# Performance work log

Measured on AMD Instinct MI355X. Metric: run time of the kernel, lower is better.

Reference implementation:

```python
import jax, jax.numpy as jnp
import numpy as np

N_NODES = 200000


def _gcn_conv(x, W, b, src, dst, n):
    # PyG GCNConv: h = D^{-1/2} (A + I) D^{-1/2} (x @ W) + b
    h = x @ W  # [N, F_out]
    deg = jax.ops.segment_sum(jnp.ones(dst.shape[0], x.dtype), dst, num_segments=n)
    dinv = jnp.where(deg > 0, jax.lax.rsqrt(deg), 0.0)  # deg_inv_sqrt, inf -> 0
    norm = dinv[src] * dinv[dst]  # [E+N]
    msg = h[src] * norm[:, None]  # gather + scale, dominant memory traffic
    out = jax.ops.segment_sum(msg, dst, num_segments=n)
    return out + b


def setup_inputs() -> dict:
    key = jax.random.key(0)
    k1, k2, k3, k4, k5, k6 = jax.random.split(key, 6)
    x = jax.random.normal(k1, (N_NODES, 1), dtype=jnp.float32)
    edge_index = jax.random.randint(k2, (2, 12800000), 0, N_NODES, dtype=jnp.int64)
    # Glorot-style init like PyG GCNConv
    W1 = jax.random.normal(k3, (1, 16), dtype=jnp.float32) * (1.0 / np.sqrt(1))
    b1 = jnp.zeros((16,), dtype=jnp.float32)
    W2 = jax.random.normal(k4, (16, 1), dtype=jnp.float32) * (1.0 / np.sqrt(16))
    b2 = jnp.zeros((1,), dtype=jnp.float32)
    return {"x": x, "edge_index": edge_index, "W1": W1, "b1": b1, "W2": W2, "b2": b2}


def reference(x, edge_index, W1, b1, W2, b2):
    n = x.shape[0]
    # add self-loops once (static edge count: E + N)
    loops = jnp.arange(n, dtype=edge_index.dtype)
    src = jnp.concatenate([edge_index[0], loops])
    dst = jnp.concatenate([edge_index[1], loops])
    h = _gcn_conv(x, W1, b1, src, dst, n)
    h = jax.nn.relu(h)
    out = _gcn_conv(h, W2, b2, src, dst, n)
    return out
```

## Files before the change

kernel.cpp:

```cpp
#include <hip/hip_runtime.h>

#define TPB 256
#define BTPB 1024
#define STPB 512
#define LOG_S 13
#define S (1 << LOG_S)
#define RMAX 32
#define CHUNK 8192
#define MAXC 40
#define SLACK 32768
#define SCALEF 2097152.0f
#define INV_SCALEF (1.0f / 2097152.0f)


__global__ void k_initcur(int* __restrict__ cur, int R, int cap) {
    int t = threadIdx.x;
    if (t < R) cur[t] = t * cap;
}

__global__ __launch_bounds__(BTPB) void k_bin(const int* __restrict__ dst,
                                              const int* __restrict__ src, int e,
                                              int R, int cap,
                                              int* __restrict__ cur,
                                              unsigned* __restrict__ bkt) {
    __shared__ unsigned stage[CHUNK];
    __shared__ int h[RMAX], lofs[RMAX + 1], gbase[RMAX];
    int t = threadIdx.x;
    int b0 = blockIdx.x * CHUNK;
    int m = min(CHUNK, e - b0);
    if (t < RMAX) h[t] = 0;
    __syncthreads();
    unsigned pack[8];
    int rr[8];
    const int4* d4p = (const int4*)(dst + b0);
    const int4* s4p = (const int4*)(src + b0);
    int m4 = m >> 2;
    #pragma unroll
    for (int g = 0; g < 2; g++) {
        int i4 = g * BTPB + t;
        if (i4 < m4) {
            int4 d = d4p[i4];
            int4 s = s4p[i4];
            #pragma unroll
            for (int k = 0; k < 4; k++) {
                int dd = (k == 0) ? d.x : (k == 1) ? d.y : (k == 2) ? d.z : d.w;
                int ss = (k == 0) ? s.x : (k == 1) ? s.y : (k == 2) ? s.z : s.w;
                int r = dd >> LOG_S;
                pack[g * 4 + k] = ((unsigned)(dd - (r << LOG_S)) << 18) | (unsigned)ss;
                int rk = atomicAdd(&h[r], 1);
                rr[g * 4 + k] = (r << 13) | rk;
            }
        } else {
            #pragma unroll
            for (int k = 0; k < 4; k++) rr[g * 4 + k] = -1;
        }
    }
    __syncthreads();
    if (t < 64) {
        int hv = (t < R) ? h[t] : 0;
        int v = hv;
        for (int o = 1; o < 64; o <<= 1) {
            int u = __shfl_up(v, o);
            if (t >= o) v += u;
        }
        if (t < R) lofs[t] = v - hv;
        if (t == R - 1) lofs[R] = v;
        if (t < R && hv > 0) gbase[t] = atomicAdd(&cur[t], hv);
    }
    __syncthreads();
    #pragma unroll
    for (int k = 0; k < 8; k++) {
        if (rr[k] >= 0)
            stage[lofs[rr[k] >> 13] + (rr[k] & 8191)] = pack[k];
    }
    __syncthreads();
    for (int j = t; j < m; j += BTPB) {
        int lo = 0, hi = R;
        while (hi - lo > 1) {
            int mid = (lo + hi) >> 1;
            if (lofs[mid] <= j) lo = mid; else hi = mid;
        }
        int gi = gbase[lo] + (j - lofs[lo]);
        if (gi < (lo + 1) * cap)
            bkt[gi] = stage[j];
    }
}

template <int MODE>
__global__ __launch_bounds__(STPB) void k_scat(const unsigned* __restrict__ bkt,
                                               const int* __restrict__ cur,
                                               int cap,
                                               const float* __restrict__ val,
                                               int* __restrict__ partials, int bpr) {
    __shared__ int acc[S];
    int t = threadIdx.x;
    int r = blockIdx.x / bpr;
    int c = blockIdx.x - r * bpr;
    int4* acc4 = (int4*)acc;
    for (int j = t; j < S / 4; j += STPB) acc4[j] = make_int4(0, 0, 0, 0);
    __syncthreads();
    const unsigned* bk = bkt + (size_t)r * cap;
    int len = min(cur[r] - r * cap, cap);
    int len4 = len >> 2;
    const uint4* bk4 = (const uint4*)bk;
    int stride = bpr * STPB;
    int i0 = c * STPB + t;
    bool h0 = i0 < len4, h1 = (i0 + stride) < len4;
    uint4 p0, p1;
    if (h0) p0 = bk4[i0];
    if (h1) p1 = bk4[i0 + stride];
    int v0x = 1, v0y = 1, v0z = 1, v0w = 1;
    if (MODE == 1 && h0) {
        v0x = (int)rintf(val[p0.x & 0x3FFFFu] * SCALEF);
        v0y = (int)rintf(val[p0.y & 0x3FFFFu] * SCALEF);
        v0z = (int)rintf(val[p0.z & 0x3FFFFu] * SCALEF);
        v0w = (int)rintf(val[p0.w & 0x3FFFFu] * SCALEF);
    }
    int inext = i0 + 2 * stride;
    while (h0) {
        uint4 p2;
        bool h2 = inext < len4;
        if (h2) p2 = bk4[inext];
        int v1x = 1, v1y = 1, v1z = 1, v1w = 1;
        if (MODE == 1 && h1) {
            v1x = (int)rintf(val[p1.x & 0x3FFFFu] * SCALEF);
            v1y = (int)rintf(val[p1.y & 0x3FFFFu] * SCALEF);
            v1z = (int)rintf(val[p1.z & 0x3FFFFu] * SCALEF);
            v1w = (int)rintf(val[p1.w & 0x3FFFFu] * SCALEF);
        }
        atomicAdd(&acc[p0.x >> 18], v0x);
        atomicAdd(&acc[p0.y >> 18], v0y);
        atomicAdd(&acc[p0.z >> 18], v0z);
        atomicAdd(&acc[p0.w >> 18], v0w);
        p0 = p1; h0 = h1;
        p1 = p2; h1 = h2;
        v0x = v1x; v0y = v1y; v0z = v1z; v0w = v1w;
        inext += stride;
    }
    for (int k = (len4 << 2) + c * STPB + t; k < len; k += stride) {
        unsigned p = bk[k];
        if (MODE == 0) atomicAdd(&acc[p >> 18], 1);
        else atomicAdd(&acc[p >> 18], (int)rintf(val[p & 0x3FFFFu] * SCALEF));
    }
    __syncthreads();
    if (MODE == 0) {
        unsigned* o16 = (unsigned*)((unsigned short*)partials + (size_t)blockIdx.x * S);
        const int2* acc2 = (const int2*)acc;
        for (int j = t; j < S / 2; j += STPB) {
            int2 a = acc2[j];
            o16[j] = (unsigned)a.x | ((unsigned)a.y << 16);
        }
    } else {
        int4* out4 = (int4*)(partials + (size_t)blockIdx.x * S);
        for (int j = t; j < S / 4; j += STPB) out4[j] = acc4[j];
    }
}

__device__ __forceinline__ int redp(const int* __restrict__ partials, int i, int bpr) {
    int r = i >> LOG_S;
    int slot = i & (S - 1);
    const int* p = partials + (size_t)r * bpr * S + slot;
    int s = 0;
    #pragma unroll 8
    for (int c = 0; c < bpr; c++) s += p[(size_t)c * S];
    return s;
}

__global__ void k_red_dinv(const int* __restrict__ partials, int bpr,
                           const float* __restrict__ x, float* __restrict__ dinv,
                           float* __restrict__ y, int n) {
    int i2 = blockIdx.x * blockDim.x + threadIdx.x;
    int i = i2 << 1;
    if (i + 1 < n) {
        int r = i >> LOG_S;
        int slot = i & (S - 1);
        const unsigned* pb = (const unsigned*)partials
                             + (size_t)r * bpr * (S / 2) + (slot >> 1);
        int s0 = 0, s1 = 0;
        #pragma unroll 8
        for (int c = 0; c < bpr; c++) {
            unsigned v = pb[(size_t)c * (S / 2)];
            s0 += (int)(v & 0xFFFFu);
            s1 += (int)(v >> 16);
        }
        float d0 = rsqrtf((float)s0 + 1.0f);
        float d1 = rsqrtf((float)s1 + 1.0f);
        float2 xx = *(const float2*)(x + i);
        *(float2*)(dinv + i) = make_float2(d0, d1);
        *(float2*)(y + i) = make_float2(xx.x * d0, xx.y * d1);
    } else if (i < n) {
        int r = i >> LOG_S;
        int slot = i & (S - 1);
        const unsigned short* pb = (const unsigned short*)partials
                                   + (size_t)r * bpr * S + slot;
        int s0 = 0;
        for (int c = 0; c < bpr; c++) s0 += (int)pb[(size_t)c * S];
        float d0 = rsqrtf((float)s0 + 1.0f);
        dinv[i] = d0;
        y[i] = x[i] * d0;
    }
}

__global__ void k_red_node(const int* __restrict__ partials, int bpr,
                           const float* __restrict__ dinv, const float* __restrict__ y,
                           float* __restrict__ z,
                           const float* __restrict__ W1, const float* __restrict__ b1,
                           const float* __restrict__ W2, int n, int f) {
    int q = blockIdx.x * blockDim.x + threadIdx.x;
    int i = q << 2;
    if (i + 3 < n) {
        int r = i >> LOG_S;
        int slot = i & (S - 1);
        const int4* p = (const int4*)(partials + (size_t)r * bpr * S + slot);
        int4 s = make_int4(0, 0, 0, 0);
        #pragma unroll 8
        for (int c = 0; c < bpr; c++) {
            int4 v = p[(size_t)c * (S / 4)];
            s.x += v.x; s.y += v.y; s.z += v.z; s.w += v.w;
        }
        float4 dv = *(const float4*)(dinv + i);
        float4 yy = *(const float4*)(y + i);
        float a0 = dv.x * ((float)s.x * INV_SCALEF + yy.x);
        float a1 = dv.y * ((float)s.y * INV_SCALEF + yy.y);
        float a2 = dv.z * ((float)s.z * INV_SCALEF + yy.z);
        float a3 = dv.w * ((float)s.w * INV_SCALEF + yy.w);
        float c0 = 0.0f, c1 = 0.0f, c2 = 0.0f, c3 = 0.0f;
        for (int j = 0; j < f; j++) {
            float w = W1[j], bb = b1[j], u = W2[j];
            c0 += fmaxf(w * a0 + bb, 0.0f) * u;
            c1 += fmaxf(w * a1 + bb, 0.0f) * u;
            c2 += fmaxf(w * a2 + bb, 0.0f) * u;
            c3 += fmaxf(w * a3 + bb, 0.0f) * u;
        }
        *(float4*)(z + i) = make_float4(c0 * dv.x, c1 * dv.y, c2 * dv.z, c3 * dv.w);
    } else {
        for (int k = i; k < n && k < i + 4; k++) {
            float num = (float)redp(partials, k, bpr) * INV_SCALEF;
            float agg = dinv[k] * (num + y[k]);
            float h2 = 0.0f;
            for (int j = 0; j < f; j++) {
                float h = W1[j] * agg + b1[j];
                h2 += fmaxf(h, 0.0f) * W2[j];
            }
            z[k] = h2 * dinv[k];
        }
    }
}

__global__ void k_red_out(const int* __restrict__ partials, int bpr,
                          const float* __restrict__ dinv, const float* __restrict__ z,
                          const float* __restrict__ b2, float* __restrict__ out, int n) {
    int q = blockIdx.x * blockDim.x + threadIdx.x;
    int i = q << 2;
    if (i + 3 < n) {
        int r = i >> LOG_S;
        int slot = i & (S - 1);
        const int4* p = (const int4*)(partials + (size_t)r * bpr * S + slot);
        int4 s = make_int4(0, 0, 0, 0);
        #pragma unroll 8
        for (int c = 0; c < bpr; c++) {
            int4 v = p[(size_t)c * (S / 4)];
            s.x += v.x; s.y += v.y; s.z += v.z; s.w += v.w;
        }
        float4 dv = *(const float4*)(dinv + i);
        float4 zz = *(const float4*)(z + i);
        float bb = b2[0];
        float4 o;
        o.x = dv.x * ((float)s.x * INV_SCALEF + zz.x) + bb;
        o.y = dv.y * ((float)s.y * INV_SCALEF + zz.y) + bb;
        o.z = dv.z * ((float)s.z * INV_SCALEF + zz.z) + bb;
        o.w = dv.w * ((float)s.w * INV_SCALEF + zz.w) + bb;
        *(float4*)(out + i) = o;
    } else {
        for (int k = i; k < n && k < i + 4; k++) {
            float num = (float)redp(partials, k, bpr) * INV_SCALEF;
            out[k] = dinv[k] * (num + z[k]) + b2[0];
        }
    }
}

__global__ void g_init(float* __restrict__ deg, float* __restrict__ num, int n) {
    int i = blockIdx.x * blockDim.x + threadIdx.x;
    if (i < n) { deg[i] = 1.0f; num[i] = 0.0f; }
}
__global__ void g_deg(const int* __restrict__ dst, float* __restrict__ deg, int e) {
    int i = blockIdx.x * blockDim.x + threadIdx.x;
    if (i < e) atomicAdd(deg + dst[i], 1.0f);
}
__global__ void g_dinv(const float* __restrict__ x, float* __restrict__ dd,
                       float* __restrict__ y, int n) {
    int i = blockIdx.x * blockDim.x + threadIdx.x;
    if (i < n) { float d = rsqrtf(dd[i]); dd[i] = d; y[i] = x[i] * d; }
}
__global__ void g_scatter(const int* __restrict__ src, const int* __restrict__ dst,
                          const float* __restrict__ val, float* __restrict__ num, int e) {
    int i = blockIdx.x * blockDim.x + threadIdx.x;
    if (i < e) atomicAdd(num + dst[i], val[src[i]]);
}
__global__ void g_node(const float* __restrict__ dinv, const float* __restrict__ y,
                       float* __restrict__ num, float* __restrict__ z,
                       const float* __restrict__ W1, const float* __restrict__ b1,
                       const float* __restrict__ W2, int n, int f) {
    int i = blockIdx.x * blockDim.x + threadIdx.x;
    if (i < n) {
        float agg = dinv[i] * (num[i] + y[i]);
        float h2 = 0.0f;
        for (int j = 0; j < f; j++) {
            float h = W1[j] * agg + b1[j];
            h2 += fmaxf(h, 0.0f) * W2[j];
        }
        z[i] = h2 * dinv[i];
        num[i] = 0.0f;
    }
}
__global__ void g_out(const float* __restrict__ dinv, const float* __restrict__ z,
                      const float* __restrict__ num, const float* __restrict__ b2,
                      float* __restrict__ out, int n) {
    int i = blockIdx.x * blockDim.x + threadIdx.x;
    if (i < n) out[i] = dinv[i] * (num[i] + z[i]) + b2[0];
}

extern "C" void kernel_launch(void* const* d_in, const int* in_sizes, int n_in,
                              void* d_out, int out_size, void* d_ws, size_t ws_size,
                              hipStream_t stream) {
    const float* x  = (const float*)d_in[0];
    const int*   ei = (const int*)d_in[1];
    const float* W1 = (const float*)d_in[2];
    const float* b1 = (const float*)d_in[3];
    const float* W2 = (const float*)d_in[4];
    const float* b2 = (const float*)d_in[5];

    int n = in_sizes[0];
    int e = in_sizes[1] / 2;
    int f = in_sizes[2];

    const int* src = ei;
    const int* dst = ei + e;
    float* out = (float*)d_out;

    int R  = (n + S - 1) >> LOG_S;
    int gn = (n + TPB - 1) / TPB;
    size_t words = ws_size / 4;

    size_t o_A   = 0;
    size_t o_B   = o_A + n;
    size_t o_D   = o_B + n;
    size_t o_cur = o_D + n;
    size_t o_bkt = (o_cur + RMAX + 3) & ~(size_t)3;
    int cap = ((e / R) + SLACK + 3) & ~3;
    size_t bkt_w = (size_t)R * cap;
    size_t o_part = o_bkt + bkt_w;

    float* A = (float*)d_ws + o_A;
    float* B = (float*)d_ws + o_B;
    float* D = (float*)d_ws + o_D;
    int*   cur = (int*)d_ws + o_cur;

    int bpr = 0;
    if (R <= RMAX && n <= (1 << 18) && words > o_part) {
        size_t per_c = (size_t)R * S;
        size_t m = (words - o_part) / per_c;
        bpr = (int)(m > MAXC ? MAXC : m);
        while (bpr > 0 && R * bpr > 1024) bpr--;
    }

    if (bpr >= 4) {
        unsigned* bkt = (unsigned*)d_ws + o_bkt;
        int* partials = (int*)d_ws + o_part;
        int gs = R * bpr;
        int gbin = (e + CHUNK - 1) / CHUNK;
        int gn2 = (((n + 1) >> 1) + TPB - 1) / TPB;
        int gn4 = (((n + 3) >> 2) + TPB - 1) / TPB;
        k_initcur<<<1, RMAX, 0, stream>>>(cur, R, cap);
        k_bin<<<gbin, BTPB, 0, stream>>>(dst, src, e, R, cap, cur, bkt);
        k_scat<0><<<gs, STPB, 0, stream>>>(bkt, cur, cap, nullptr, partials, bpr);
        k_red_dinv<<<gn2, TPB, 0, stream>>>(partials, bpr, x, A, B, n);
        k_scat<1><<<gs, STPB, 0, stream>>>(bkt, cur, cap, B, partials, bpr);
        k_red_node<<<gn4, TPB, 0, stream>>>(partials, bpr, A, B, D, W1, b1, W2, n, f);
        k_scat<1><<<gs, STPB, 0, stream>>>(bkt, cur, cap, D, partials, bpr);
        k_red_out<<<gn4, TPB, 0, stream>>>(partials, bpr, A, D, b2, out, n);
    } else {
        float* C = D + n;
        int ge = (e + TPB - 1) / TPB;
        g_init<<<gn, TPB, 0, stream>>>(A, C, n);
        g_deg<<<ge, TPB, 0, stream>>>(dst, A, e);
        g_dinv<<<gn, TPB, 0, stream>>>(x, A, B, n);
        g_scatter<<<ge, TPB, 0, stream>>>(src, dst, B, C, e);
        g_node<<<gn, TPB, 0, stream>>>(A, B, C, D, W1, b1, W2, n, f);
        g_scatter<<<ge, TPB, 0, stream>>>(src, dst, D, C, e);
        g_out<<<gn, TPB, 0, stream>>>(A, D, C, b2, out, n);
    }
}
```

Before: 328.6 us.

## Halve per-range scatter blocks and use scalar per-node reduction kernels

Lowers the cap on scatter blocks per bucket range from 40 to 20, which halves the partial histograms each reducer must sum but gives the scatter phase less parallelism. The node and output reduction kernels drop the int4/float4 four-nodes-per-thread path and use one node per thread with the scalar redp helper. Reduce loop unroll factors rise to 20 to match. The scalar path uses narrower loads but launches more threads to hide latency.

```diff
diff --git a/kernel.cpp b/kernel.cpp
--- a/kernel.cpp
+++ b/kernel.cpp
@@ -7,7 +7,7 @@
 #define S (1 << LOG_S)
 #define RMAX 32
 #define CHUNK 8192
-#define MAXC 40
+#define MAXC 20
 #define SLACK 32768
 #define SCALEF 2097152.0f
 #define INV_SCALEF (1.0f / 2097152.0f)
@@ -161,7 +161,7 @@
     int slot = i & (S - 1);
     const int* p = partials + (size_t)r * bpr * S + slot;
     int s = 0;
-    #pragma unroll 8
+    #pragma unroll 20
     for (int c = 0; c < bpr; c++) s += p[(size_t)c * S];
     return s;
 }
@@ -177,7 +177,7 @@
         const unsigned* pb = (const unsigned*)partials
                              + (size_t)r * bpr * (S / 2) + (slot >> 1);
         int s0 = 0, s1 = 0;
-        #pragma unroll 8
+        #pragma unroll 20
         for (int c = 0; c < bpr; c++) {
             unsigned v = pb[(size_t)c * (S / 2)];
             s0 += (int)(v & 0xFFFFu);
@@ -206,76 +206,27 @@
                            float* __restrict__ z,
                            const float* __restrict__ W1, const float* __restrict__ b1,
                            const float* __restrict__ W2, int n, int f) {
-    int q = blockIdx.x * blockDim.x + threadIdx.x;
-    int i = q << 2;
-    if (i + 3 < n) {
-        int r = i >> LOG_S;
-        int slot = i & (S - 1);
-        const int4* p = (const int4*)(partials + (size_t)r * bpr * S + slot);
-        int4 s = make_int4(0, 0, 0, 0);
-        #pragma unroll 8
-        for (int c = 0; c < bpr; c++) {
-            int4 v = p[(size_t)c * (S / 4)];
-            s.x += v.x; s.y += v.y; s.z += v.z; s.w += v.w;
-        }
-        float4 dv = *(const float4*)(dinv + i);
-        float4 yy = *(const float4*)(y + i);
-        float a0 = dv.x * ((float)s.x * INV_SCALEF + yy.x);
-        float a1 = dv.y * ((float)s.y * INV_SCALEF + yy.y);
-        float a2 = dv.z * ((float)s.z * INV_SCALEF + yy.z);
-        float a3 = dv.w * ((float)s.w * INV_SCALEF + yy.w);
-        float c0 = 0.0f, c1 = 0.0f, c2 = 0.0f, c3 = 0.0f;
+    int i = blockIdx.x * blockDim.x + threadIdx.x;
+    if (i < n) {
+        float num = (float)redp(partials, i, bpr) * INV_SCALEF;
+        float dv = dinv[i];
+        float agg = dv * (num + y[i]);
+        float h2 = 0.0f;
         for (int j = 0; j < f; j++) {
-            float w = W1[j], bb = b1[j], u = W2[j];
-            c0 += fmaxf(w * a0 + bb, 0.0f) * u;
-            c1 += fmaxf(w * a1 + bb, 0.0f) * u;
-            c2 += fmaxf(w * a2 + bb, 0.0f) * u;
-            c3 += fmaxf(w * a3 + bb, 0.0f) * u;
-        }
-        *(float4*)(z + i) = make_float4(c0 * dv.x, c1 * dv.y, c2 * dv.z, c3 * dv.w);
-    } else {
-        for (int k = i; k < n && k < i + 4; k++) {
-            float num = (float)redp(partials, k, bpr) * INV_SCALEF;
-            float agg = dinv[k] * (num + y[k]);
-            float h2 = 0.0f;
-            for (int j = 0; j < f; j++) {
-                float h = W1[j] * agg + b1[j];
-                h2 += fmaxf(h, 0.0f) * W2[j];
-            }
-            z[k] = h2 * dinv[k];
-        }
+            float h = W1[j] * agg + b1[j];
+            h2 += fmaxf(h, 0.0f) * W2[j];
+        }
+        z[i] = h2 * dv;
     }
 }
 
 __global__ void k_red_out(const int* __restrict__ partials, int bpr,
                           const float* __restrict__ dinv, const float* __restrict__ z,
                           const float* __restrict__ b2, float* __restrict__ out, int n) {
-    int q = blockIdx.x * blockDim.x + threadIdx.x;
-    int i = q << 2;
-    if (i + 3 < n) {
-        int r = i >> LOG_S;
-        int slot = i & (S - 1);
-        const int4* p = (const int4*)(partials + (size_t)r * bpr * S + slot);
-        int4 s = make_int4(0, 0, 0, 0);
-        #pragma unroll 8
-        for (int c = 0; c < bpr; c++) {
-            int4 v = p[(size_t)c * (S / 4)];
-            s.x += v.x; s.y += v.y; s.z += v.z; s.w += v.w;
-        }
-        float4 dv = *(const float4*)(dinv + i);
-        float4 zz = *(const float4*)(z + i);
-        float bb = b2[0];
-        float4 o;
-        o.x = dv.x * ((float)s.x * INV_SCALEF + zz.x) + bb;
-        o.y = dv.y * ((float)s.y * INV_SCALEF + zz.y) + bb;
-        o.z = dv.z * ((float)s.z * INV_SCALEF + zz.z) + bb;
-        o.w = dv.w * ((float)s.w * INV_SCALEF + zz.w) + bb;
-        *(float4*)(out + i) = o;
-    } else {
-        for (int k = i; k < n && k < i + 4; k++) {
-            float num = (float)redp(partials, k, bpr) * INV_SCALEF;
-            out[k] = dinv[k] * (num + z[k]) + b2[0];
-        }
+    int i = blockIdx.x * blockDim.x + threadIdx.x;
+    if (i < n) {
+        float num = (float)redp(partials, i, bpr) * INV_SCALEF;
+        out[i] = dinv[i] * (num + z[i]) + b2[0];
     }
 }
 
@@ -370,15 +321,14 @@
         int gs = R * bpr;
         int gbin = (e + CHUNK - 1) / CHUNK;
         int gn2 = (((n + 1) >> 1) + TPB - 1) / TPB;
-        int gn4 = (((n + 3) >> 2) + TPB - 1) / TPB;
         k_initcur<<<1, RMAX, 0, stream>>>(cur, R, cap);
         k_bin<<<gbin, BTPB, 0, stream>>>(dst, src, e, R, cap, cur, bkt);
         k_scat<0><<<gs, STPB, 0, stream>>>(bkt, cur, cap, nullptr, partials, bpr);
         k_red_dinv<<<gn2, TPB, 0, stream>>>(partials, bpr, x, A, B, n);
         k_scat<1><<<gs, STPB, 0, stream>>>(bkt, cur, cap, B, partials, bpr);
-        k_red_node<<<gn4, TPB, 0, stream>>>(partials, bpr, A, B, D, W1, b1, W2, n, f);
+        k_red_node<<<gn, TPB, 0, stream>>>(partials, bpr, A, B, D, W1, b1, W2, n, f);
         k_scat<1><<<gs, STPB, 0, stream>>>(bkt, cur, cap, D, partials, bpr);
-        k_red_out<<<gn4, TPB, 0, stream>>>(partials, bpr, A, D, b2, out, n);
+        k_red_out<<<gn, TPB, 0, stream>>>(partials, bpr, A, D, b2, out, n);
     } else {
         float* C = D + n;
         int ge = (e + TPB - 1) / TPB;
```

Measured after the change: 327.4 us. About the same (-0.4%).
